# Kernel optimization log

Measured on AMD Instinct MI355X. Metric: run time of the kernel, lower is better.

Reference implementation:

```python
import jax, jax.numpy as jnp
import numpy as np

B, S, D = 4, 2048, 768
H, E = 12, 64  # num_heads, head_size


def setup_inputs() -> dict:
    key = jax.random.key(0)
    ks = jax.random.split(key, 9)
    sd = 1.0 / np.sqrt(D)
    return {
        "x": jax.random.normal(ks[0], (B, S, D), dtype=jnp.float32),
        "Wq": jax.random.normal(ks[1], (H, D, E), dtype=jnp.float32) * sd,
        "bq": jax.random.normal(ks[2], (H, E), dtype=jnp.float32) * 0.02,
        "Wk": jax.random.normal(ks[3], (H, D, E), dtype=jnp.float32) * sd,
        "bk": jax.random.normal(ks[4], (H, E), dtype=jnp.float32) * 0.02,
        "Wv": jax.random.normal(ks[5], (H, D, E), dtype=jnp.float32) * sd,
        "bv": jax.random.normal(ks[6], (H, E), dtype=jnp.float32) * 0.02,
        "Wp": jax.random.normal(ks[7], (H * E, D), dtype=jnp.float32) * sd,
        "bp": jax.random.normal(ks[8], (D,), dtype=jnp.float32) * 0.02,
    }


def reference(x, Wq, bq, Wk, bk, Wv, bv, Wp, bp):
    # Batched multi-head QKV projections (replaces per-head Python loop)
    q = jnp.einsum("bsd,hde->bhse", x, Wq) + bq[None, :, None, :]
    k = jnp.einsum("bsd,hde->bhse", x, Wk) + bk[None, :, None, :]
    v = jnp.einsum("bsd,hde->bhse", x, Wv) + bv[None, :, None, :]
    scale = 1.0 / jnp.sqrt(jnp.asarray(E, dtype=x.dtype))
    # Full materialized attention matrix [B,H,S,S] as in the original module
    wei = jnp.einsum("bhqe,bhke->bhqk", q, k) * scale
    wei = jax.nn.softmax(wei, axis=-1)  # dropout=0 (eval) => identity
    out = jnp.einsum("bhqk,bhke->bhqe", wei, v)  # [B,H,S,E]
    # concat heads in head order then output projection
    out = out.transpose(0, 2, 1, 3).reshape(B, S, H * E)
    return out @ Wp + bp
```

## Files before the change

kernel.cpp:

```cpp
#include <hip/hip_runtime.h>
#include <cstddef>
#include <cstdint>

#define NB 4
#define NH 12
#define SQ 2048
#define DM 768
#define EH 64
#define MTOT (NB*SQ)
#define NQKV (NH*3*EH)

typedef __attribute__((ext_vector_type(8))) short short8;
typedef __attribute__((ext_vector_type(4))) float floatx4;

#define QSCALE 0.18033688011112042f

__device__ __forceinline__ unsigned short f2bf(float f) {
    unsigned int u = __float_as_uint(f);
    u += 0x7fffu + ((u >> 16) & 1u);
    return (unsigned short)(u >> 16);
}

#if __has_builtin(__builtin_amdgcn_cvt_pk_bf16_f32)
typedef __attribute__((ext_vector_type(2))) __bf16 bf16x2_t;
__device__ __forceinline__ unsigned int pack_bf16(float lo, float hi) {
    bf16x2_t v = __builtin_amdgcn_cvt_pk_bf16_f32(lo, hi);
    return __builtin_bit_cast(unsigned int, v);
}
#else
__device__ __forceinline__ unsigned int pack_bf16(float lo, float hi) {
    unsigned int u0 = __float_as_uint(lo) + 0x8000u;
    unsigned int u1 = __float_as_uint(hi) + 0x8000u;
    return __builtin_amdgcn_perm(u1, u0, 0x07060302u);
}
#endif
__device__ __forceinline__ short8 pack8(float a0,float a1,float a2,float a3,
                                        float b0,float b1,float b2,float b3) {
    union { unsigned int u[4]; short8 s; } cv;
    cv.u[0] = pack_bf16(a0, a1);
    cv.u[1] = pack_bf16(a2, a3);
    cv.u[2] = pack_bf16(b0, b1);
    cv.u[3] = pack_bf16(b2, b3);
    return cv.s;
}
__device__ __forceinline__ void gl_lds16(const void* g, void* l) {
    __builtin_amdgcn_global_load_lds(
        (const __attribute__((address_space(1))) unsigned int*)g,
        (__attribute__((address_space(3))) unsigned int*)l, 16, 0, 0);
}

#define CVT_A 1572864
#define CVT_B (CVT_A + 442368)
#define CVT_C (CVT_B + 147456)
#define CVT_D (CVT_C + 576)
__global__ __launch_bounds__(256) void convert_pack(
    const float* __restrict__ x,
    const float* __restrict__ Wq, const float* __restrict__ bq,
    const float* __restrict__ Wk, const float* __restrict__ bk,
    const float* __restrict__ Wv, const float* __restrict__ bv,
    const float* __restrict__ Wp,
    unsigned short* __restrict__ Xb, unsigned short* __restrict__ Wt,
    unsigned short* __restrict__ Wpt, float* __restrict__ bias_all)
{
    int t = blockIdx.x * 256 + threadIdx.x;
    if (t < CVT_A) {
        float4 v = ((const float4*)x)[t];
        ushort4 r; r.x = f2bf(v.x); r.y = f2bf(v.y); r.z = f2bf(v.z); r.w = f2bf(v.w);
        ((ushort4*)Xb)[t] = r;
    } else if (t < CVT_B) {
        int u = t - CVT_A;
        int n = u / 192, kc = (u % 192) * 4;
        int h = n / 192, rr = n % 192, wsel = rr >> 6, e = rr & 63;
        const float* W = (wsel == 0) ? Wq : ((wsel == 1) ? Wk : Wv);
        float sc = (wsel == 0) ? QSCALE : 1.0f;
        ushort4 r;
        r.x = f2bf(W[((size_t)h * DM + kc + 0) * EH + e] * sc);
        r.y = f2bf(W[((size_t)h * DM + kc + 1) * EH + e] * sc);
        r.z = f2bf(W[((size_t)h * DM + kc + 2) * EH + e] * sc);
        r.w = f2bf(W[((size_t)h * DM + kc + 3) * EH + e] * sc);
        ((ushort4*)Wt)[u] = r;
    } else if (t < CVT_C) {
        int u = t - CVT_B;
        int n = u / 192, kc = (u % 192) * 4;
        ushort4 r;
        r.x = f2bf(Wp[(size_t)(kc + 0) * DM + n]);
        r.y = f2bf(Wp[(size_t)(kc + 1) * DM + n]);
        r.z = f2bf(Wp[(size_t)(kc + 2) * DM + n]);
        r.w = f2bf(Wp[(size_t)(kc + 3) * DM + n]);
        ((ushort4*)Wpt)[u] = r;
    } else if (t < CVT_D) {
        int u = (t - CVT_C) * 4;
        #pragma unroll
        for (int j = 0; j < 4; j++) {
            int n = u + j;
            int h = n / 192, rr = n % 192, wsel = rr >> 6, e = rr & 63;
            const float* bs = (wsel == 0) ? bq : ((wsel == 1) ? bk : bv);
            bias_all[n] = bs[h * EH + e] * ((wsel == 0) ? QSCALE : 1.0f);
        }
    }
}

__global__ __launch_bounds__(256) void qkv_mfma(
    const unsigned short* __restrict__ Xb, const unsigned short* __restrict__ Wt,
    const float* __restrict__ bias_all,
    unsigned short* __restrict__ Qo, unsigned short* __restrict__ Kf,
    unsigned short* __restrict__ Vf)
{
    __shared__ unsigned short As[128 * 32];
    __shared__ unsigned short Bs[128 * 32];
    __shared__ unsigned short Ep[4][16 * 72];
    const int tid = threadIdx.x;
    const int w = tid >> 6, lane = tid & 63;
    const int l15 = lane & 15, quad = lane >> 4;
    const int wm = w & 1, wn = w >> 1;
    const int m0 = blockIdx.x * 128, n0 = blockIdx.y * 128;
    const int srow = w * 32 + (lane >> 2);
    const int pchunk = lane & 3;

    floatx4 acc[4][4];
    #pragma unroll
    for (int i = 0; i < 4; i++)
        #pragma unroll
        for (int j = 0; j < 4; j++) acc[i][j] = 0;

    for (int k0 = 0; k0 < DM; k0 += 32) {
        __syncthreads();
        #pragma unroll
        for (int c = 0; c < 2; c++) {
            int mr = srow + c * 16;
            int j = (pchunk - (mr >> 1)) & 3;
            gl_lds16(&Xb[(size_t)(m0 + mr) * DM + k0 + j * 8],
                     &As[w * 1024 + c * 512 + lane * 8]);
            gl_lds16(&Wt[(size_t)(n0 + mr) * DM + k0 + j * 8],
                     &Bs[w * 1024 + c * 512 + lane * 8]);
        }
        __syncthreads();
        short8 af[4], bf[4];
        #pragma unroll
        for (int mi = 0; mi < 4; mi++) {
            int row = wm * 64 + mi * 16 + l15;
            int pp = (quad + (row >> 1)) & 3;
            af[mi] = *(const short8*)&As[row * 32 + pp * 8];
        }
        #pragma unroll
        for (int ni = 0; ni < 4; ni++) {
            int row = wn * 64 + ni * 16 + l15;
            int pp = (quad + (row >> 1)) & 3;
            bf[ni] = *(const short8*)&Bs[row * 32 + pp * 8];
        }
        #pragma unroll
        for (int mi = 0; mi < 4; mi++)
            #pragma unroll
            for (int ni = 0; ni < 4; ni++)
                acc[mi][ni] = __builtin_amdgcn_mfma_f32_16x16x32_bf16(
                    af[mi], bf[ni], acc[mi][ni], 0, 0, 0);
    }

    const int bB = m0 >> 11;
    const int ntb0 = n0 + wn * 64;
    const int h = ntb0 / 192, rr = ntb0 % 192;
    const int wsel = rr >> 6;
    const size_t bhbase = ((size_t)bB * NH + h) * (SQ * EH);
    const int sb_base = (m0 & 2047) + wm * 64;
    unsigned short* Ew = &Ep[w][0];
    float bvv[4];
    #pragma unroll
    for (int ni = 0; ni < 4; ni++) bvv[ni] = bias_all[ntb0 + ni * 16 + l15];

    if (wsel == 0) {
        #pragma unroll
        for (int mi = 0; mi < 4; mi++) {
            #pragma unroll
            for (int ni = 0; ni < 4; ni++)
                #pragma unroll
                for (int r = 0; r < 4; r++)
                    Ew[(quad * 4 + r) * 72 + ni * 16 + l15] =
                        f2bf(acc[mi][ni][r] + bvv[ni]);
            #pragma unroll
            for (int t = 0; t < 2; t++) {
                uint4 d = *(uint4*)&Ew[(t * 8 + (lane >> 3)) * 72 + (lane & 7) * 8];
                *(uint4*)&Qo[bhbase +
                    (size_t)(sb_base + mi * 16 + t * 8 + (lane >> 3)) * EH +
                    (lane & 7) * 8] = d;
            }
        }
    } else if (wsel == 1) {
        size_t tbase = bhbase + (size_t)(sb_base >> 6) * 4096;
        #pragma unroll
        for (int mi = 0; mi < 4; mi++) {
            #pragma unroll
            for (int ni = 0; ni < 4; ni++)
                #pragma unroll
                for (int r = 0; r < 4; r++)
                    Ew[(quad * 4 + r) * 72 + ni * 16 + l15] =
                        f2bf(acc[mi][ni][r] + bvv[ni]);
            #pragma unroll
            for (int t = 0; t < 2; t++) {
                uint4 d = *(uint4*)&Ew[l15 * 72 + t * 32 + quad * 8];
                *(uint4*)&Kf[tbase +
                    (size_t)((mi * 2 + t) * 64 + quad * 16 + l15) * 8] = d;
            }
        }
    } else {
        size_t tbase = bhbase + (size_t)(sb_base >> 6) * 4096;
        #pragma unroll
        for (int ni = 0; ni < 4; ni++) {
            #pragma unroll
            for (int mi = 0; mi < 4; mi++)
                #pragma unroll
                for (int r = 0; r < 4; r += 2) {
                    unsigned int pr = pack_bf16(acc[mi][ni][r]     + bvv[ni],
                                                acc[mi][ni][r + 1] + bvv[ni]);
                    *(unsigned int*)&Ew[l15 * 72 + quad * 16 + mi * 4 + r] = pr;
                }
            #pragma unroll
            for (int t = 0; t < 2; t++) {
                uint4 d = *(uint4*)&Ew[l15 * 72 + t * 32 + quad * 8];
                int unit = (ni * 2 + (quad & 1)) * 64 + ((quad >> 1) + 2 * t) * 16 + l15;
                *(uint4*)&Vf[tbase + (size_t)unit * 8] = d;
            }
        }
    }
}

__global__ __launch_bounds__(256, 3) void attn_mfma(
    const unsigned short* __restrict__ Q, const unsigned short* __restrict__ Kf,
    const unsigned short* __restrict__ Vf, unsigned short* __restrict__ O)
{
    __shared__ unsigned short Ks[2][4096];
    __shared__ unsigned short Vs[2][4096];
    const int tid = threadIdx.x;
    const int w = tid >> 6, lane = tid & 63;
    const int l15 = lane & 15, quad = lane >> 4;
    const int bh = blockIdx.x;
    const int b = bh / NH, h = bh % NH;
    const int q0 = blockIdx.y * 128;

    const unsigned short* Qb = Q + (size_t)bh * SQ * EH;
    const unsigned short* Kb = Kf + (size_t)bh * SQ * EH;
    const unsigned short* Vb = Vf + (size_t)bh * SQ * EH;

    short8 qf[2][2];
    #pragma unroll
    for (int qh = 0; qh < 2; qh++)
        #pragma unroll
        for (int kh = 0; kh < 2; kh++)
            qf[qh][kh] = *(const short8*)
                &Qb[(size_t)(q0 + w * 32 + qh * 16 + l15) * EH + kh * 32 + quad * 8];

    short8 ones;
    #pragma unroll
    for (int j = 0; j < 8; j++) ones[j] = (short)0x3F80;

    floatx4 o[2][4], l_acc[2];
    #pragma unroll
    for (int qh = 0; qh < 2; qh++) {
        l_acc[qh] = 0;
        #pragma unroll
        for (int nb = 0; nb < 4; nb++) o[qh][nb] = 0;
    }

    const int seg = w * 2;
    #pragma unroll
    for (int c = 0; c < 2; c++) {
        gl_lds16(&Kb[(seg + c) * 512 + lane * 8], &Ks[0][(seg + c) * 512 + lane * 8]);
        gl_lds16(&Vb[(seg + c) * 512 + lane * 8], &Vs[0][(seg + c) * 512 + lane * 8]);
    }

    #pragma unroll 2
    for (int kb = 0; kb < SQ / 64; kb++) {
        const int cur = kb & 1;
        __syncthreads();
        if (kb + 1 < SQ / 64) {
            const unsigned short* Kn = Kb + (size_t)(kb + 1) * 4096;
            const unsigned short* Vn = Vb + (size_t)(kb + 1) * 4096;
            #pragma unroll
            for (int c = 0; c < 2; c++) {
                gl_lds16(&Kn[(seg + c) * 512 + lane * 8],
                         &Ks[cur ^ 1][(seg + c) * 512 + lane * 8]);
                gl_lds16(&Vn[(seg + c) * 512 + lane * 8],
                         &Vs[cur ^ 1][(seg + c) * 512 + lane * 8]);
            }
        }
        short8 kf[4][2];
        #pragma unroll
        for (int nb = 0; nb < 4; nb++)
            #pragma unroll
            for (int kh = 0; kh < 2; kh++)
                kf[nb][kh] = *(const short8*)&Ks[cur][((nb * 2 + kh) * 64 + lane) * 8];
        floatx4 s[2][4];
        #pragma unroll
        for (int qh = 0; qh < 2; qh++)
            #pragma unroll
            for (int nb = 0; nb < 4; nb++) {
                floatx4 z = 0;
                z = __builtin_amdgcn_mfma_f32_16x16x32_bf16(kf[nb][0], qf[qh][0], z, 0, 0, 0);
                z = __builtin_amdgcn_mfma_f32_16x16x32_bf16(kf[nb][1], qf[qh][1], z, 0, 0, 0);
                s[qh][nb] = z;
            }
        short8 pa[2][2];
        #pragma unroll
        for (int qh = 0; qh < 2; qh++) {
            float p[4][4];
            #pragma unroll
            for (int nb = 0; nb < 4; nb++)
                #pragma unroll
                for (int r = 0; r < 4; r++)
                    p[nb][r] = exp2f(s[qh][nb][r]);
            pa[qh][0] = pack8(p[0][0], p[0][1], p[0][2], p[0][3],
                              p[1][0], p[1][1], p[1][2], p[1][3]);
            pa[qh][1] = pack8(p[2][0], p[2][1], p[2][2], p[2][3],
                              p[3][0], p[3][1], p[3][2], p[3][3]);
            l_acc[qh] = __builtin_amdgcn_mfma_f32_16x16x32_bf16(pa[qh][0], ones, l_acc[qh], 0, 0, 0);
            l_acc[qh] = __builtin_amdgcn_mfma_f32_16x16x32_bf16(pa[qh][1], ones, l_acc[qh], 0, 0, 0);
        }
        short8 vf[4][2];
        #pragma unroll
        for (int eb = 0; eb < 4; eb++)
            #pragma unroll
            for (int kh = 0; kh < 2; kh++)
                vf[eb][kh] = *(const short8*)&Vs[cur][((eb * 2 + kh) * 64 + lane) * 8];
        #pragma unroll
        for (int qh = 0; qh < 2; qh++)
            #pragma unroll
            for (int eb = 0; eb < 4; eb++) {
                o[qh][eb] = __builtin_amdgcn_mfma_f32_16x16x32_bf16(pa[qh][0], vf[eb][0], o[qh][eb], 0, 0, 0);
                o[qh][eb] = __builtin_amdgcn_mfma_f32_16x16x32_bf16(pa[qh][1], vf[eb][1], o[qh][eb], 0, 0, 0);
            }
    }

    #pragma unroll
    for (int qh = 0; qh < 2; qh++)
        #pragma unroll
        for (int r = 0; r < 4; r++) {
            float inv = 1.0f / l_acc[qh][r];
            int sidx = q0 + w * 32 + qh * 16 + quad * 4 + r;
            size_t base = (((size_t)b * SQ + sidx) * NH + h) * EH + l15;
            O[base +  0] = f2bf(o[qh][0][r] * inv);
            O[base + 16] = f2bf(o[qh][1][r] * inv);
            O[base + 32] = f2bf(o[qh][2][r] * inv);
            O[base + 48] = f2bf(o[qh][3][r] * inv);
        }
}

__global__ __launch_bounds__(256) void proj_mfma(
    const unsigned short* __restrict__ Ab, const unsigned short* __restrict__ Wpt,
    const float* __restrict__ bp, float* __restrict__ C)
{
    __shared__ unsigned short As[64 * 32];
    __shared__ unsigned short Bs[128 * 32];
    __shared__ float Epf[4][16 * 68];
    const int tid = threadIdx.x;
    const int w = tid >> 6, lane = tid & 63;
    const int l15 = lane & 15, quad = lane >> 4;
    const int wm = w & 1, wn = w >> 1;
    const int m0 = blockIdx.x * 64, n0 = blockIdx.y * 128;
    const int pchunk = lane & 3;

    floatx4 acc[2][4];
    #pragma unroll
    for (int i = 0; i < 2; i++)
        #pragma unroll
        for (int j = 0; j < 4; j++) acc[i][j] = 0;

    for (int k0 = 0; k0 < DM; k0 += 32) {
        __syncthreads();
        {
            int mr = w * 16 + (lane >> 2);
            int j = (pchunk - (mr >> 1)) & 3;
            gl_lds16(&Ab[(size_t)(m0 + mr) * DM + k0 + j * 8], &As[w * 512 + lane * 8]);
        }
        #pragma unroll
        for (int c = 0; c < 2; c++) {
            int nr = w * 32 + c * 16 + (lane >> 2);
            int j = (pchunk - (nr >> 1)) & 3;
            gl_lds16(&Wpt[(size_t)(n0 + nr) * DM + k0 + j * 8],
                     &Bs[w * 1024 + c * 512 + lane * 8]);
        }
        __syncthreads();
        short8 af[2], bf[4];
        #pragma unroll
        for (int mi = 0; mi < 2; mi++) {
            int row = wm * 32 + mi * 16 + l15;
            int pp = (quad + (row >> 1)) & 3;
            af[mi] = *(const short8*)&As[row * 32 + pp * 8];
        }
        #pragma unroll
        for (int ni = 0; ni < 4; ni++) {
            int row = wn * 64 + ni * 16 + l15;
            int pp = (quad + (row >> 1)) & 3;
            bf[ni] = *(const short8*)&Bs[row * 32 + pp * 8];
        }
        #pragma unroll
        for (int mi = 0; mi < 2; mi++)
            #pragma unroll
            for (int ni = 0; ni < 4; ni++)
                acc[mi][ni] = __builtin_amdgcn_mfma_f32_16x16x32_bf16(
                    af[mi], bf[ni], acc[mi][ni], 0, 0, 0);
    }

    float* Ewf = &Epf[w][0];
    float bvv[4];
    #pragma unroll
    for (int ni = 0; ni < 4; ni++) bvv[ni] = bp[n0 + wn * 64 + ni * 16 + l15];
    #pragma unroll
    for (int mi = 0; mi < 2; mi++) {
        #pragma unroll
        for (int ni = 0; ni < 4; ni++)
            #pragma unroll
            for (int r = 0; r < 4; r++)
                Ewf[(quad * 4 + r) * 68 + ni * 16 + l15] = acc[mi][ni][r] + bvv[ni];
        #pragma unroll
        for (int t = 0; t < 4; t++) {
            float4 d = *(float4*)&Ewf[(t * 4 + quad) * 68 + l15 * 4];
            *(float4*)&C[(size_t)(m0 + wm * 32 + mi * 16 + t * 4 + quad) * DM +
                         n0 + wn * 64 + l15 * 4] = d;
        }
    }
}

extern "C" void kernel_launch(void* const* d_in, const int* in_sizes, int n_in,
                              void* d_out, int out_size, void* d_ws, size_t ws_size,
                              hipStream_t stream) {
    const float* x  = (const float*)d_in[0];
    const float* Wq = (const float*)d_in[1];
    const float* bq = (const float*)d_in[2];
    const float* Wk = (const float*)d_in[3];
    const float* bk = (const float*)d_in[4];
    const float* Wv = (const float*)d_in[5];
    const float* bv = (const float*)d_in[6];
    const float* Wp = (const float*)d_in[7];
    const float* bp = (const float*)d_in[8];
    float* out = (float*)d_out;

    const size_t QKV_ELEMS = (size_t)NB * NH * SQ * EH;
    unsigned short* Qb   = (unsigned short*)d_ws;
    unsigned short* Kfb  = Qb + QKV_ELEMS;
    unsigned short* Vfb  = Kfb + QKV_ELEMS;
    unsigned short* Abuf = Vfb + QKV_ELEMS;
    unsigned short* Xb   = Abuf + QKV_ELEMS;
    unsigned short* Wtb  = Xb + QKV_ELEMS;
    unsigned short* Wptb = Wtb + (size_t)NQKV * DM;
    float* bias_all      = (float*)(Wptb + (size_t)DM * DM);

    convert_pack<<<(CVT_D + 255) / 256, 256, 0, stream>>>(
        x, Wq, bq, Wk, bk, Wv, bv, Wp, Xb, Wtb, Wptb, bias_all);
    qkv_mfma<<<dim3(MTOT / 128, NQKV / 128), 256, 0, stream>>>(
        Xb, Wtb, bias_all, Qb, Kfb, Vfb);
    attn_mfma<<<dim3(NB * NH, SQ / 128), 256, 0, stream>>>(Qb, Kfb, Vfb, Abuf);
    proj_mfma<<<dim3(MTOT / 64, DM / 128), 256, 0, stream>>>(Abuf, Wptb, bp, out);
}
```

Baseline: 244.9 us.

## Double-buffer LDS tiles in QKV and projection GEMMs; use hardware exp2 in attention

The QKV and output-projection GEMM main loops now keep two LDS buffers per operand. The next K-slice's global-to-LDS loads are issued before the current slice is read, so each iteration needs one barrier instead of two and load latency overlaps with MFMA work. The attention softmax calls the raw hardware exp2 builtin instead of exp2f, which drops libm range and denormal handling. The first QK MFMA now takes a constant zero accumulator. The cost is doubled LDS use in the GEMMs, which may lower occupancy, and slightly different exp2 behaviour for extreme inputs.

Measured after the change: 230.1 us. 6.0% less time.

```diff
diff --git a/kernel.cpp b/kernel.cpp
--- a/kernel.cpp
+++ b/kernel.cpp
@@ -20,6 +20,12 @@
     u += 0x7fffu + ((u >> 16) & 1u);
     return (unsigned short)(u >> 16);
 }
+
+#if __has_builtin(__builtin_amdgcn_exp2f)
+__device__ __forceinline__ float fast_exp2(float x) { return __builtin_amdgcn_exp2f(x); }
+#else
+__device__ __forceinline__ float fast_exp2(float x) { return exp2f(x); }
+#endif
 
 #if __has_builtin(__builtin_amdgcn_cvt_pk_bf16_f32)
 typedef __attribute__((ext_vector_type(2))) __bf16 bf16x2_t;
@@ -106,8 +112,8 @@
     unsigned short* __restrict__ Qo, unsigned short* __restrict__ Kf,
     unsigned short* __restrict__ Vf)
 {
-    __shared__ unsigned short As[128 * 32];
-    __shared__ unsigned short Bs[128 * 32];
+    __shared__ unsigned short As[2][128 * 32];
+    __shared__ unsigned short Bs[2][128 * 32];
     __shared__ unsigned short Ep[4][16 * 72];
     const int tid = threadIdx.x;
     const int w = tid >> 6, lane = tid & 63;
@@ -123,30 +129,43 @@
         #pragma unroll
         for (int j = 0; j < 4; j++) acc[i][j] = 0;
 
-    for (int k0 = 0; k0 < DM; k0 += 32) {
+    #pragma unroll
+    for (int c = 0; c < 2; c++) {
+        int mr = srow + c * 16;
+        int j = (pchunk - (mr >> 1)) & 3;
+        gl_lds16(&Xb[(size_t)(m0 + mr) * DM + j * 8],
+                 &As[0][w * 1024 + c * 512 + lane * 8]);
+        gl_lds16(&Wt[(size_t)(n0 + mr) * DM + j * 8],
+                 &Bs[0][w * 1024 + c * 512 + lane * 8]);
+    }
+
+    for (int kt = 0; kt < DM / 32; kt++) {
+        const int cur = kt & 1;
         __syncthreads();
-        #pragma unroll
-        for (int c = 0; c < 2; c++) {
-            int mr = srow + c * 16;
-            int j = (pchunk - (mr >> 1)) & 3;
-            gl_lds16(&Xb[(size_t)(m0 + mr) * DM + k0 + j * 8],
-                     &As[w * 1024 + c * 512 + lane * 8]);
-            gl_lds16(&Wt[(size_t)(n0 + mr) * DM + k0 + j * 8],
-                     &Bs[w * 1024 + c * 512 + lane * 8]);
-        }
-        __syncthreads();
+        if (kt + 1 < DM / 32) {
+            int k0n = (kt + 1) * 32;
+            #pragma unroll
+            for (int c = 0; c < 2; c++) {
+                int mr = srow + c * 16;
+                int j = (pchunk - (mr >> 1)) & 3;
+                gl_lds16(&Xb[(size_t)(m0 + mr) * DM + k0n + j * 8],
+                         &As[cur ^ 1][w * 1024 + c * 512 + lane * 8]);
+                gl_lds16(&Wt[(size_t)(n0 + mr) * DM + k0n + j * 8],
+                         &Bs[cur ^ 1][w * 1024 + c * 512 + lane * 8]);
+            }
+        }
         short8 af[4], bf[4];
         #pragma unroll
         for (int mi = 0; mi < 4; mi++) {
             int row = wm * 64 + mi * 16 + l15;
             int pp = (quad + (row >> 1)) & 3;
-            af[mi] = *(const short8*)&As[row * 32 + pp * 8];
+            af[mi] = *(const short8*)&As[cur][row * 32 + pp * 8];
         }
         #pragma unroll
         for (int ni = 0; ni < 4; ni++) {
             int row = wn * 64 + ni * 16 + l15;
             int pp = (quad + (row >> 1)) & 3;
-            bf[ni] = *(const short8*)&Bs[row * 32 + pp * 8];
+            bf[ni] = *(const short8*)&Bs[cur][row * 32 + pp * 8];
         }
         #pragma unroll
         for (int mi = 0; mi < 4; mi++)
@@ -155,6 +174,7 @@
                 acc[mi][ni] = __builtin_amdgcn_mfma_f32_16x16x32_bf16(
                     af[mi], bf[ni], acc[mi][ni], 0, 0, 0);
     }
+    __syncthreads();
 
     const int bB = m0 >> 11;
     const int ntb0 = n0 + wn * 64;
@@ -251,6 +271,7 @@
     short8 ones;
     #pragma unroll
     for (int j = 0; j < 8; j++) ones[j] = (short)0x3F80;
+    const floatx4 fzero = 0;
 
     floatx4 o[2][4], l_acc[2];
     #pragma unroll
@@ -293,10 +314,10 @@
         for (int qh = 0; qh < 2; qh++)
             #pragma unroll
             for (int nb = 0; nb < 4; nb++) {
-                floatx4 z = 0;
-                z = __builtin_amdgcn_mfma_f32_16x16x32_bf16(kf[nb][0], qf[qh][0], z, 0, 0, 0);
-                z = __builtin_amdgcn_mfma_f32_16x16x32_bf16(kf[nb][1], qf[qh][1], z, 0, 0, 0);
-                s[qh][nb] = z;
+                floatx4 z = __builtin_amdgcn_mfma_f32_16x16x32_bf16(
+                    kf[nb][0], qf[qh][0], fzero, 0, 0, 0);
+                s[qh][nb] = __builtin_amdgcn_mfma_f32_16x16x32_bf16(
+                    kf[nb][1], qf[qh][1], z, 0, 0, 0);
             }
         short8 pa[2][2];
         #pragma unroll
@@ -306,7 +327,7 @@
             for (int nb = 0; nb < 4; nb++)
                 #pragma unroll
                 for (int r = 0; r < 4; r++)
-                    p[nb][r] = exp2f(s[qh][nb][r]);
+                    p[nb][r] = fast_exp2(s[qh][nb][r]);
             pa[qh][0] = pack8(p[0][0], p[0][1], p[0][2], p[0][3],
                               p[1][0], p[1][1], p[1][2], p[1][3]);
             pa[qh][1] = pack8(p[2][0], p[2][1], p[2][2], p[2][3],
@@ -347,8 +368,8 @@
     const unsigned short* __restrict__ Ab, const unsigned short* __restrict__ Wpt,
     const float* __restrict__ bp, float* __restrict__ C)
 {
-    __shared__ unsigned short As[64 * 32];
-    __shared__ unsigned short Bs[128 * 32];
+    __shared__ unsigned short As[2][64 * 32];
+    __shared__ unsigned short Bs[2][128 * 32];
     __shared__ float Epf[4][16 * 68];
     const int tid = threadIdx.x;
     const int w = tid >> 6, lane = tid & 63;
@@ -363,33 +384,50 @@
         #pragma unroll
         for (int j = 0; j < 4; j++) acc[i][j] = 0;
 
-    for (int k0 = 0; k0 < DM; k0 += 32) {
+    {
+        int mr = w * 16 + (lane >> 2);
+        int j = (pchunk - (mr >> 1)) & 3;
+        gl_lds16(&Ab[(size_t)(m0 + mr) * DM + j * 8], &As[0][w * 512 + lane * 8]);
+    }
+    #pragma unroll
+    for (int c = 0; c < 2; c++) {
+        int nr = w * 32 + c * 16 + (lane >> 2);
+        int j = (pchunk - (nr >> 1)) & 3;
+        gl_lds16(&Wpt[(size_t)(n0 + nr) * DM + j * 8],
+                 &Bs[0][w * 1024 + c * 512 + lane * 8]);
+    }
+
+    for (int kt = 0; kt < DM / 32; kt++) {
+        const int cur = kt & 1;
         __syncthreads();
-        {
-            int mr = w * 16 + (lane >> 2);
-            int j = (pchunk - (mr >> 1)) & 3;
-            gl_lds16(&Ab[(size_t)(m0 + mr) * DM + k0 + j * 8], &As[w * 512 + lane * 8]);
-        }
-        #pragma unroll
-        for (int c = 0; c < 2; c++) {
-            int nr = w * 32 + c * 16 + (lane >> 2);
-            int j = (pchunk - (nr >> 1)) & 3;
-            gl_lds16(&Wpt[(size_t)(n0 + nr) * DM + k0 + j * 8],
-                     &Bs[w * 1024 + c * 512 + lane * 8]);
-        }
-        __syncthreads();
+        if (kt + 1 < DM / 32) {
+            int k0n = (kt + 1) * 32;
+            {
+                int mr = w * 16 + (lane >> 2);
+                int j = (pchunk - (mr >> 1)) & 3;
+                gl_lds16(&Ab[(size_t)(m0 + mr) * DM + k0n + j * 8],
+                         &As[cur ^ 1][w * 512 + lane * 8]);
+            }
+            #pragma unroll
+            for (int c = 0; c < 2; c++) {
+                int nr = w * 32 + c * 16 + (lane >> 2);
+                int j = (pchunk - (nr >> 1)) & 3;
+                gl_lds16(&Wpt[(size_t)(n0 + nr) * DM + k0n + j * 8],
+                         &Bs[cur ^ 1][w * 1024 + c * 512 + lane * 8]);
+            }
+        }
         short8 af[2], bf[4];
         #pragma unroll
         for (int mi = 0; mi < 2; mi++) {
             int row = wm * 32 + mi * 16 + l15;
             int pp = (quad + (row >> 1)) & 3;
-            af[mi] = *(const short8*)&As[row * 32 + pp * 8];
+            af[mi] = *(const short8*)&As[cur][row * 32 + pp * 8];
         }
         #pragma unroll
         for (int ni = 0; ni < 4; ni++) {
             int row = wn * 64 + ni * 16 + l15;
             int pp = (quad + (row >> 1)) & 3;
-            bf[ni] = *(const short8*)&Bs[row * 32 + pp * 8];
+            bf[ni] = *(const short8*)&Bs[cur][row * 32 + pp * 8];
         }
         #pragma unroll
         for (int mi = 0; mi < 2; mi++)
@@ -398,6 +436,7 @@
                 acc[mi][ni] = __builtin_amdgcn_mfma_f32_16x16x32_bf16(
                     af[mi], bf[ni], acc[mi][ni], 0, 0, 0);
     }
+    __syncthreads();
 
     float* Ewf = &Epf[w][0];
     float bvv[4];
```
